# Performance work log

Hardware: AMD Instinct MI355X
Metric: run time of the kernel (lower is better)

## Reference

```python
import jax, jax.numpy as jnp
import numpy as np

D_PROJ = 256
SCALE = D_PROJ ** (-0.5)
NEG_INF = -1e30  # stands in for float('-inf'); avoids NaN-prone -inf arithmetic


def setup_inputs() -> dict:
    key = jax.random.key(0)
    kH, kG, kM, kWk, kWq = jax.random.split(key, 5)
    B, L, T, Dh, Dg = 8, 2048, 1024, 1024, 768
    H = jax.random.normal(kH, (B, L, Dh), dtype=jnp.float32)
    G = jax.random.normal(kG, (B, T, Dg), dtype=jnp.float32)
    mask = jax.random.randint(kM, (B, L), 0, 2).astype(bool)  # True = masked
    Wk = jax.random.normal(kWk, (D_PROJ, Dh), dtype=jnp.float32) * (Dh ** -0.5)
    Wq = jax.random.normal(kWq, (D_PROJ, Dg), dtype=jnp.float32) * (Dg ** -0.5)
    return {"H": H, "G": G, "mask": mask, "Wk": Wk, "Wq": Wq}


def reference(H, G, mask, Wk, Wq):
    # K = Wk(H): (B, L, P); Q = Wq(G): (B, T, P)
    K = jnp.einsum("bld,pd->blp", H, Wk)
    Q = jnp.einsum("btd,pd->btp", G, Wq)
    # logits: (B, T, L), scaled dot product
    logits = jnp.einsum("btp,blp->btl", Q, K) * SCALE
    logits = jnp.where(mask[:, None, :], NEG_INF, logits)
    # softmax in fp32 over L (original casts logits to fp32 before softmax)
    alpha = jax.nn.softmax(logits.astype(jnp.float32), axis=-1).astype(H.dtype)
    # Z = alpha @ H: (B, T, Dh)
    Z = jnp.einsum("btl,bld->btd", alpha, H)
    return Z
```

## Files before the change

### kernel.cpp

```cpp
#include <hip/hip_runtime.h>
#include <hip/hip_bf16.h>

typedef short s16x8 __attribute__((ext_vector_type(8)));
typedef float f32x4 __attribute__((ext_vector_type(4)));
typedef unsigned short u16x8 __attribute__((ext_vector_type(8)));

__device__ __forceinline__ unsigned short f2bf(float f) {
  union { __hip_bfloat16 h; unsigned short u; } cv;
  cv.h = __float2bfloat16(f);
  return cv.u;
}
__device__ __forceinline__ float bf2f(unsigned short u) {
  union { unsigned int i; float f; } cv;
  cv.i = ((unsigned int)u) << 16;
  return cv.f;
}

__device__ __forceinline__ void gload_lds16(const void* g, void* l) {
  __builtin_amdgcn_global_load_lds(
      (const __attribute__((address_space(1))) unsigned int*)g,
      (__attribute__((address_space(3))) unsigned int*)l,
      16, 0, 0);
}

__global__ __launch_bounds__(256) void prep(
    const float* __restrict__ G, unsigned short* __restrict__ Gbf,
    const float* __restrict__ Wk, unsigned short* __restrict__ Wkbf,
    const float* __restrict__ Wq, unsigned short* __restrict__ Wqbf,
    const int* __restrict__ mask, int* __restrict__ idx,
    int* __restrict__ Lc, int* __restrict__ Lcp) {
  const int t = threadIdx.x;
  if (blockIdx.x >= 1024) {
    const int b = blockIdx.x - 1024;
    const int* mb = mask + (size_t)b * 2048;
    int* ib = idx + (size_t)b * 2048;
    __shared__ int tot[256];
    __shared__ int off[257];
    int keep[8], cnt = 0;
#pragma unroll
    for (int j = 0; j < 8; ++j) {
      keep[j] = (mb[t * 8 + j] == 0);
      cnt += keep[j];
    }
    tot[t] = cnt;
    __syncthreads();
    if (t == 0) {
      int s = 0;
      for (int i = 0; i < 256; ++i) { off[i] = s; s += tot[i]; }
      off[256] = s;
    }
    __syncthreads();
    int p = off[t];
#pragma unroll
    for (int j = 0; j < 8; ++j)
      if (keep[j]) ib[p++] = t * 8 + j;
    if (t == 0) {
      Lc[b] = off[256];
      Lcp[b] = (off[256] + 127) & ~127;
    }
    return;
  }
  const int n4a = 8 * 1024 * 768 / 4, n4b = 256 * 1024 / 4, n4c = 256 * 768 / 4;
  const int total = n4a + n4b + n4c;
  for (int i = blockIdx.x * 256 + t; i < total; i += 1024 * 256) {
    const float* s; unsigned short* d; int j = i;
    if (j < n4a) { s = G; d = Gbf; }
    else if ((j -= n4a) < n4b) { s = Wk; d = Wkbf; }
    else { j -= n4b; s = Wq; d = Wqbf; }
    float4 v = *(const float4*)(s + (size_t)j * 4);
    ushort4 o;
    o.x = f2bf(v.x); o.y = f2bf(v.y); o.z = f2bf(v.z); o.w = f2bf(v.w);
    *(ushort4*)(d + (size_t)j * 4) = o;
  }
}

__global__ __launch_bounds__(256) void gather_cast(
    const float* __restrict__ H, const int* __restrict__ idx,
    const int* __restrict__ Lc, const int* __restrict__ Lcp,
    unsigned short* __restrict__ Hc, unsigned short* __restrict__ HcT) {
  const int b = blockIdx.z;
  const int j0 = blockIdx.x * 64, d0 = blockIdx.y * 64;
  if (j0 >= Lcp[b]) return;
  const int lc = Lc[b];
  __shared__ unsigned short tile[64][72];
  const int t = threadIdx.x;

  const int r = t >> 2, dc = (t & 3) * 16;
  const int j = j0 + r;
  const int src = (j < lc) ? idx[(size_t)b * 2048 + j] : -1;
  ushort4 s[4];
  if (src >= 0) {
    const float* p = H + ((size_t)b * 2048 + src) * 1024 + d0 + dc;
#pragma unroll
    for (int i = 0; i < 4; ++i) {
      float4 v = *(const float4*)(p + 4 * i);
      s[i].x = f2bf(v.x); s[i].y = f2bf(v.y); s[i].z = f2bf(v.z); s[i].w = f2bf(v.w);
    }
  } else {
#pragma unroll
    for (int i = 0; i < 4; ++i) { s[i].x = 0; s[i].y = 0; s[i].z = 0; s[i].w = 0; }
  }
  unsigned short* hcrow = Hc + ((size_t)b * 2048 + j) * 1024 + d0 + dc;
#pragma unroll
  for (int i = 0; i < 4; ++i) {
    *(ushort4*)&tile[r][dc + 4 * i] = s[i];
    *(ushort4*)(hcrow + 4 * i) = s[i];
  }
  __syncthreads();

  const int dr = t >> 2, lcc = (t & 3) * 16;
  unsigned short o[16];
#pragma unroll
  for (int i = 0; i < 16; ++i) o[i] = tile[lcc + i][dr];
  unsigned short* dst = HcT + ((size_t)b * 1024 + d0 + dr) * 2048 + j0 + lcc;
  *(uint4*)dst = *(uint4*)&o[0];
  *(uint4*)(dst + 8) = *(uint4*)&o[8];
}

template <int BN, int EPI, bool OUT_BF16>
__device__ __forceinline__ void gemm_core(
    unsigned short* As, unsigned short* Bs, float* redLds,
    const unsigned short* __restrict__ Abf, const unsigned short* __restrict__ Bbf,
    void* __restrict__ Cg_, int N, int K, int lda, int ldb, float scale,
    int bm, int bn, int lcv, float* __restrict__ psumOut,
    const float* __restrict__ psumB, int nb) {
  constexpr int NF = BN / 32;
  const int tid = threadIdx.x;
  const int l = tid & 63, wid = tid >> 6;
  const int wr = wid >> 1, wc = wid & 1;
  const int rowA0 = bm * 128, rowB0 = bn * BN;

  const int srow = l >> 3;
  const int sslot = (l & 7) ^ (srow & 7);
  const int soff = sslot * 8;

  if constexpr (EPI == 2) {
    if (tid < 128) {
      float s = 0.f;
      for (int j = 0; j < nb; ++j) s += psumB[(size_t)j * 1024 + tid];
      redLds[tid] = 1.0f / s;
    }
  }

  f32x4 acc[4][NF] = {};

  for (int k0 = 0; k0 < K; k0 += 64) {
#pragma unroll
    for (int i = 0; i < 4; ++i) {
      const int c = wid * 4 + i;
      gload_lds16(Abf + (size_t)(rowA0 + c * 8 + srow) * lda + k0 + soff,
                  &As[c * 512]);
    }
#pragma unroll
    for (int i = 0; i < BN / 32; ++i) {
      const int c = wid * (BN / 32) + i;
      gload_lds16(Bbf + (size_t)(rowB0 + c * 8 + srow) * ldb + k0 + soff,
                  &Bs[c * 512]);
    }
    __syncthreads();

    s16x8 af[4][2], bfr[NF][2];
#pragma unroll
    for (int m = 0; m < 4; ++m) {
      const int row = wr * 64 + m * 16 + (l & 15);
      const int rx = row & 7;
#pragma unroll
      for (int kk = 0; kk < 2; ++kk) {
        const int slot = kk * 4 + (l >> 4);
        af[m][kk] = *(const s16x8*)&As[row * 64 + (slot ^ rx) * 8];
      }
    }
#pragma unroll
    for (int n = 0; n < NF; ++n) {
      const int row = wc * (BN / 2) + n * 16 + (l & 15);
      const int rx = row & 7;
#pragma unroll
      for (int kk = 0; kk < 2; ++kk) {
        const int slot = kk * 4 + (l >> 4);
        bfr[n][kk] = *(const s16x8*)&Bs[row * 64 + (slot ^ rx) * 8];
      }
    }
#pragma unroll
    for (int kk = 0; kk < 2; ++kk)
#pragma unroll
      for (int m = 0; m < 4; ++m)
#pragma unroll
        for (int n = 0; n < NF; ++n)
          acc[m][n] = __builtin_amdgcn_mfma_f32_16x16x32_bf16(
              af[m][kk], bfr[n][kk], acc[m][n], 0, 0, 0);
    __syncthreads();
  }

  const int crow0 = bm * 128 + wr * 64, ccol0 = bn * BN + wc * (BN / 2);
  unsigned short* Cst = (unsigned short*)Cg_;
  float* Cf = (float*)Cg_;

  if constexpr (EPI == 1) {
    float (*psumLds)[128] = (float(*)[128])redLds;
    float rs[4][4];
#pragma unroll
    for (int m = 0; m < 4; ++m)
#pragma unroll
      for (int r = 0; r < 4; ++r) rs[m][r] = 0.f;
#pragma unroll
    for (int m = 0; m < 4; ++m) {
#pragma unroll
      for (int n = 0; n < NF; ++n) {
#pragma unroll
        for (int r = 0; r < 4; ++r) {
          const int row = crow0 + m * 16 + ((l >> 4) << 2) + r;
          const int col = ccol0 + n * 16 + (l & 15);
          const float e = (col < lcv) ? __expf(acc[m][n][r] * scale) : 0.f;
          rs[m][r] += e;
          Cst[(size_t)row * N + col] = f2bf(e);
        }
      }
    }
#pragma unroll
    for (int m = 0; m < 4; ++m)
#pragma unroll
      for (int r = 0; r < 4; ++r) {
#pragma unroll
        for (int off = 1; off < 16; off <<= 1)
          rs[m][r] += __shfl_xor(rs[m][r], off);
      }
    if ((l & 15) == 0) {
      const int q = l >> 4;
#pragma unroll
      for (int m = 0; m < 4; ++m)
#pragma unroll
        for (int r = 0; r < 4; ++r)
          psumLds[wc][wr * 64 + m * 16 + q * 4 + r] = rs[m][r];
    }
    __syncthreads();
    if (tid < 128)
      psumOut[tid] = psumLds[0][tid] + psumLds[1][tid];
  } else {
#pragma unroll
    for (int m = 0; m < 4; ++m) {
#pragma unroll
      for (int n = 0; n < NF; ++n) {
#pragma unroll
        for (int r = 0; r < 4; ++r) {
          const int rloc = wr * 64 + m * 16 + ((l >> 4) << 2) + r;
          const int row = bm * 128 + rloc;
          const int col = ccol0 + n * 16 + (l & 15);
          float val = acc[m][n][r] * scale;
          if constexpr (EPI == 2) val *= redLds[rloc];
          if constexpr (OUT_BF16)
            Cst[(size_t)row * N + col] = f2bf(val);
          else
            Cf[(size_t)row * N + col] = val;
        }
      }
    }
  }
}

__global__ __launch_bounds__(256) void gemm_kqproj(
    const unsigned short* __restrict__ Hc, const unsigned short* __restrict__ Wkbf,
    unsigned short* __restrict__ Kc,
    const unsigned short* __restrict__ Gbf, const unsigned short* __restrict__ Wqbf,
    unsigned short* __restrict__ Qbuf, const int* __restrict__ Lcp) {
  __shared__ unsigned short As[128 * 64];
  __shared__ unsigned short Bs[64 * 64];
  __shared__ float redLds[256];
  int x = blockIdx.x;
  const unsigned short *A_, *B_;
  unsigned short* C_;
  int K_, ld_, bm, bn;
  if (x < 512) {
    const int b = x & 7, inner = x >> 3;
    bm = inner >> 2; bn = inner & 3;
    if (bm * 128 >= Lcp[b]) return;
    A_ = Hc + (size_t)b * 2048 * 1024;
    B_ = Wkbf;
    C_ = Kc + (size_t)b * 2048 * 256;
    K_ = 1024; ld_ = 1024;
  } else {
    x -= 512;
    const int logical = (x & 7) * 32 + (x >> 3);
    bm = logical >> 2; bn = logical & 3;
    A_ = Gbf; B_ = Wqbf; C_ = Qbuf;
    K_ = 768; ld_ = 768;
  }
  gemm_core<64, 0, true>(As, Bs, redLds, A_, B_, C_, 256, K_, ld_, ld_, 1.0f,
                         bm, bn, 0, nullptr, nullptr, 0);
}

__global__ __launch_bounds__(256) void gemm_score(
    const unsigned short* __restrict__ Qbuf, const unsigned short* __restrict__ Kc,
    unsigned short* __restrict__ Sbuf, const int* __restrict__ Lcp,
    const int* __restrict__ Lc, float* __restrict__ Psum) {
  __shared__ unsigned short As[128 * 64];
  __shared__ unsigned short Bs[128 * 64];
  __shared__ float redLds[256];
  const int b = blockIdx.x & 7, inner = blockIdx.x >> 3;
  const int bm = inner >> 4, bn = inner & 15;
  if (bn * 128 >= Lcp[b]) return;
  gemm_core<128, 1, true>(
      As, Bs, redLds,
      Qbuf + (size_t)b * 1024 * 256, Kc + (size_t)b * 2048 * 256,
      Sbuf + (size_t)b * 1024 * 2048, 2048, 256, 256, 256, 0.0625f,
      bm, bn, Lc[b], Psum + ((size_t)b * 16 + bn) * 1024 + bm * 128,
      nullptr, 0);
}

__global__ __launch_bounds__(256) void gemm_pv(
    const unsigned short* __restrict__ Sbuf, const unsigned short* __restrict__ HcT,
    float* __restrict__ Z, const int* __restrict__ Lcp,
    const float* __restrict__ Psum) {
  __shared__ unsigned short As[128 * 64];
  __shared__ unsigned short Bs[128 * 64];
  __shared__ float redLds[256];
  const int b = blockIdx.x & 7, inner = blockIdx.x >> 3;
  const int bm = inner >> 3, bn = inner & 7;
  const int K = Lcp[b], nb = K >> 7;
  gemm_core<128, 2, false>(
      As, Bs, redLds,
      Sbuf + (size_t)b * 1024 * 2048, HcT + (size_t)b * 1024 * 2048,
      Z + (size_t)b * 1024 * 1024, 1024, K, 2048, 2048, 1.0f,
      bm, bn, 0, nullptr, Psum + (size_t)b * 16 * 1024 + bm * 128, nb);
}

extern "C" void kernel_launch(void* const* d_in, const int* in_sizes, int n_in,
                              void* d_out, int out_size, void* d_ws, size_t ws_size,
                              hipStream_t stream) {
  const float* H  = (const float*)d_in[0];
  const float* G  = (const float*)d_in[1];
  const int* mask = (const int*)d_in[2];
  const float* Wk = (const float*)d_in[3];
  const float* Wq = (const float*)d_in[4];
  float* Z = (float*)d_out;

  const size_t MiB = 1024 * 1024;
  char* ws = (char*)d_ws;
  unsigned short* HcT  = (unsigned short*)(ws);
  unsigned short* Hc   = (unsigned short*)(ws + 32 * MiB);
  unsigned short* Sbuf = Hc;
  unsigned short* Kc   = (unsigned short*)(ws + 64 * MiB);
  unsigned short* Qbuf = (unsigned short*)(ws + 72 * MiB);
  int* idx = (int*)Qbuf;
  int* Lc  = (int*)(ws + 76 * MiB);
  int* Lcp = Lc + 16;
  unsigned short* Gbf  = (unsigned short*)(ws + 76 * MiB + 4096);
  unsigned short* Wkbf = (unsigned short*)(ws + 89 * MiB);
  unsigned short* Wqbf = (unsigned short*)(ws + 90 * MiB);
  float* PsumBuf = (float*)(ws + 91 * MiB);

  prep<<<dim3(1032), 256, 0, stream>>>(G, Gbf, Wk, Wkbf, Wq, Wqbf,
                                       mask, idx, Lc, Lcp);

  gather_cast<<<dim3(32, 16, 8), 256, 0, stream>>>(H, idx, Lc, Lcp, Hc, HcT);

  gemm_kqproj<<<dim3(768), 256, 0, stream>>>(Hc, Wkbf, Kc, Gbf, Wqbf, Qbuf, Lcp);

  gemm_score<<<dim3(1024), 256, 0, stream>>>(Qbuf, Kc, Sbuf, Lcp, Lc, PsumBuf);

  gemm_pv<<<dim3(512), 256, 0, stream>>>(Sbuf, HcT, Z, Lcp, PsumBuf);
}
```

Measured before the change: 88.48 us.

## Fuse mask compaction and H gather-cast into prep kernel with wave-scan

Merges the prep and gather_cast launches into one kernel. Each gather block recomputes the per-batch mask prefix scan locally with a wave-shuffle scan and builds its own 64-entry index list in shared memory, so no global idx array or cross-kernel dependency is needed. This removes one launch and the serial single-thread scan, and lets the G/W casts overlap with the gather. In exchange every gather block redundantly reads 2048 mask entries and runs a scan.

Result: faster. 85.17 us (-3.7%).

```diff
diff --git a/kernel.cpp b/kernel.cpp
--- a/kernel.cpp
+++ b/kernel.cpp
@@ -23,77 +23,106 @@
       16, 0, 0);
 }
 
-__global__ __launch_bounds__(256) void prep(
+__device__ __forceinline__ int block_excl_scan(int cnt, int* wsum, int* total) {
+  const int t = threadIdx.x;
+  const int lane = t & 63, w = t >> 6;
+  int x = cnt;
+#pragma unroll
+  for (int d = 1; d < 64; d <<= 1) {
+    int y = __shfl_up(x, d);
+    if (lane >= d) x += y;
+  }
+  if (lane == 63) wsum[w] = x;
+  __syncthreads();
+  int woff = 0;
+#pragma unroll
+  for (int i = 0; i < 4; ++i)
+    if (i < w) woff += wsum[i];
+  *total = wsum[0] + wsum[1] + wsum[2] + wsum[3];
+  return woff + x - cnt;
+}
+
+__global__ __launch_bounds__(256) void prep_gather(
+    const float* __restrict__ H, const int* __restrict__ mask,
+    int* __restrict__ Lc, int* __restrict__ Lcp,
+    unsigned short* __restrict__ Hc, unsigned short* __restrict__ HcT,
     const float* __restrict__ G, unsigned short* __restrict__ Gbf,
     const float* __restrict__ Wk, unsigned short* __restrict__ Wkbf,
-    const float* __restrict__ Wq, unsigned short* __restrict__ Wqbf,
-    const int* __restrict__ mask, int* __restrict__ idx,
-    int* __restrict__ Lc, int* __restrict__ Lcp) {
+    const float* __restrict__ Wq, unsigned short* __restrict__ Wqbf) {
   const int t = threadIdx.x;
-  if (blockIdx.x >= 1024) {
-    const int b = blockIdx.x - 1024;
+  const int flat = blockIdx.x;
+
+  if (flat >= 4104) {
+    const int cb = flat - 4104;
+    const int n4a = 8 * 1024 * 768 / 4, n4b = 256 * 1024 / 4, n4c = 256 * 768 / 4;
+    const int total = n4a + n4b + n4c;
+    for (int i = cb * 256 + t; i < total; i += 1024 * 256) {
+      const float* s; unsigned short* d; int j = i;
+      if (j < n4a) { s = G; d = Gbf; }
+      else if ((j -= n4a) < n4b) { s = Wk; d = Wkbf; }
+      else { j -= n4b; s = Wq; d = Wqbf; }
+      float4 v = *(const float4*)(s + (size_t)j * 4);
+      ushort4 o;
+      o.x = f2bf(v.x); o.y = f2bf(v.y); o.z = f2bf(v.z); o.w = f2bf(v.w);
+      *(ushort4*)(d + (size_t)j * 4) = o;
+    }
+    return;
+  }
+
+  __shared__ int wsum[4];
+
+  if (flat >= 4096) {
+    const int b = flat - 4096;
     const int* mb = mask + (size_t)b * 2048;
-    int* ib = idx + (size_t)b * 2048;
-    __shared__ int tot[256];
-    __shared__ int off[257];
-    int keep[8], cnt = 0;
-#pragma unroll
-    for (int j = 0; j < 8; ++j) {
-      keep[j] = (mb[t * 8 + j] == 0);
-      cnt += keep[j];
-    }
-    tot[t] = cnt;
-    __syncthreads();
+    int cnt = 0;
+#pragma unroll
+    for (int j = 0; j < 8; ++j) cnt += (mb[t * 8 + j] == 0);
+    int total;
+    block_excl_scan(cnt, wsum, &total);
     if (t == 0) {
-      int s = 0;
-      for (int i = 0; i < 256; ++i) { off[i] = s; s += tot[i]; }
-      off[256] = s;
-    }
-    __syncthreads();
-    int p = off[t];
-#pragma unroll
-    for (int j = 0; j < 8; ++j)
-      if (keep[j]) ib[p++] = t * 8 + j;
-    if (t == 0) {
-      Lc[b] = off[256];
-      Lcp[b] = (off[256] + 127) & ~127;
+      Lc[b] = total;
+      Lcp[b] = (total + 127) & ~127;
     }
     return;
   }
-  const int n4a = 8 * 1024 * 768 / 4, n4b = 256 * 1024 / 4, n4c = 256 * 768 / 4;
-  const int total = n4a + n4b + n4c;
-  for (int i = blockIdx.x * 256 + t; i < total; i += 1024 * 256) {
-    const float* s; unsigned short* d; int j = i;
-    if (j < n4a) { s = G; d = Gbf; }
-    else if ((j -= n4a) < n4b) { s = Wk; d = Wkbf; }
-    else { j -= n4b; s = Wq; d = Wqbf; }
-    float4 v = *(const float4*)(s + (size_t)j * 4);
-    ushort4 o;
-    o.x = f2bf(v.x); o.y = f2bf(v.y); o.z = f2bf(v.z); o.w = f2bf(v.w);
-    *(ushort4*)(d + (size_t)j * 4) = o;
-  }
-}
-
-__global__ __launch_bounds__(256) void gather_cast(
-    const float* __restrict__ H, const int* __restrict__ idx,
-    const int* __restrict__ Lc, const int* __restrict__ Lcp,
-    unsigned short* __restrict__ Hc, unsigned short* __restrict__ HcT) {
-  const int b = blockIdx.z;
-  const int j0 = blockIdx.x * 64, d0 = blockIdx.y * 64;
-  if (j0 >= Lcp[b]) return;
-  const int lc = Lc[b];
+
+  const int b = flat & 7;
+  const int inner = flat >> 3;
+  const int j0 = (inner & 31) * 64, d0 = (inner >> 5) * 64;
+
+  const int* mb = mask + (size_t)b * 2048;
+  int keep[8], cnt = 0;
+#pragma unroll
+  for (int j = 0; j < 8; ++j) {
+    keep[j] = (mb[t * 8 + j] == 0);
+    cnt += keep[j];
+  }
+  int total;
+  int p = block_excl_scan(cnt, wsum, &total);
+  const int lcp = (total + 127) & ~127;
+  if (j0 >= lcp) return;
+  const int lc = total;
+
+  __shared__ int lidx[64];
+#pragma unroll
+  for (int j = 0; j < 8; ++j) {
+    if (keep[j]) {
+      if (p >= j0 && p < j0 + 64) lidx[p - j0] = t * 8 + j;
+      ++p;
+    }
+  }
   __shared__ unsigned short tile[64][72];
-  const int t = threadIdx.x;
+  __syncthreads();
 
   const int r = t >> 2, dc = (t & 3) * 16;
   const int j = j0 + r;
-  const int src = (j < lc) ? idx[(size_t)b * 2048 + j] : -1;
+  const int src = (j < lc) ? lidx[r] : -1;
   ushort4 s[4];
   if (src >= 0) {
-    const float* p = H + ((size_t)b * 2048 + src) * 1024 + d0 + dc;
+    const float* pp = H + ((size_t)b * 2048 + src) * 1024 + d0 + dc;
 #pragma unroll
     for (int i = 0; i < 4; ++i) {
-      float4 v = *(const float4*)(p + 4 * i);
+      float4 v = *(const float4*)(pp + 4 * i);
       s[i].x = f2bf(v.x); s[i].y = f2bf(v.y); s[i].z = f2bf(v.z); s[i].w = f2bf(v.w);
     }
   } else {
@@ -340,7 +369,6 @@
   unsigned short* Sbuf = Hc;
   unsigned short* Kc   = (unsigned short*)(ws + 64 * MiB);
   unsigned short* Qbuf = (unsigned short*)(ws + 72 * MiB);
-  int* idx = (int*)Qbuf;
   int* Lc  = (int*)(ws + 76 * MiB);
   int* Lcp = Lc + 16;
   unsigned short* Gbf  = (unsigned short*)(ws + 76 * MiB + 4096);
@@ -348,10 +376,8 @@
   unsigned short* Wqbf = (unsigned short*)(ws + 90 * MiB);
   float* PsumBuf = (float*)(ws + 91 * MiB);
 
-  prep<<<dim3(1032), 256, 0, stream>>>(G, Gbf, Wk, Wkbf, Wq, Wqbf,
-                                       mask, idx, Lc, Lcp);
-
-  gather_cast<<<dim3(32, 16, 8), 256, 0, stream>>>(H, idx, Lc, Lcp, Hc, HcT);
+  prep_gather<<<dim3(5128), 256, 0, stream>>>(
+      H, mask, Lc, Lcp, Hc, HcT, G, Gbf, Wk, Wkbf, Wq, Wqbf);
 
   gemm_kqproj<<<dim3(768), 256, 0, stream>>>(Hc, Wkbf, Kc, Gbf, Wqbf, Qbuf, Lcp);
 
```
